# Optimization experiments

Hardware: AMD Instinct MI355X
Metric: run time of the kernel (lower is better)

## Reference

```python
import jax, jax.numpy as jnp
import numpy as np

T, N = 24, 2048
INPUT_DIM, HIDDEN, MEDIATE, SOCIAL, OUT_DIM = 2, 64, 128, 64, 2
N_SIZE = 2
CELL = 0.3
T_OBS, T_PRED = 9, 19
WIN = (N_SIZE + 1) ** 2  # (N_size+1)^2 = 9 window cells


def _social_pool(h, coords, mask):
    """Faithful social pooling for N_size=2, grid_cell_size=0.3.

    torch builds a dynamic grid, scatter-adds every agent's h into its cell,
    then gathers grid[int(x-R):int(x+R), int(y-R):int(y+R)] per agent.
    With R=0.3 and integer positions >= 4 (guaranteed by the margin), that
    slice is exactly the single cell (x-1, y-1), broadcast over the 3x3
    window. We compute it as a pairwise match without materializing a grid.
    Runs under torch.no_grad() -> stop_gradient.
    """
    margin = 2 * N_SIZE * CELL
    lt = jnp.stack([coords[:, 0].min(), coords[:, 1].min()]) - margin
    p = jnp.floor((coords - lt) / CELL).astype(jnp.int32)            # [N,2]
    p = p * mask.astype(jnp.int32)[:, None]                          # masked agents -> cell (0,0)
    q = p - 1                                                        # gathered cell per agent
    match = (p[None, :, 0] == q[:, None, 0]) & (p[None, :, 1] == q[:, None, 1])  # [i,j]
    cell_val = match.astype(h.dtype) @ h                             # [N,hidden] scatter-add + gather
    Hf = jnp.tile(cell_val, (1, WIN)) * mask[:, None]                # broadcast over 3x3 window, flat
    return jax.lax.stop_gradient(Hf)


def _forward(X, part_masks, all_h_t, all_c_t, Y, W_in, b_in, W_soc, b_soc,
             W_ih, W_hh, b_ih, b_hh, W_out, b_out, T_obs, T_pred):
    relu = jax.nn.relu  # dropout_prob = 0 -> Phi == ReLU

    def lstm(z, h, c):
        g = z @ W_ih.T + b_ih + h @ W_hh.T + b_hh
        i, f, gg, o = jnp.split(g, 4, axis=1)
        c = jax.nn.sigmoid(f) * c + jax.nn.sigmoid(i) * jnp.tanh(gg)
        h = jax.nn.sigmoid(o) * jnp.tanh(c)
        return h, c

    def cell_out(r, h, c, coords, m):
        Hf = _social_pool(h, coords, m)
        e = relu(Hf @ W_soc.T + b_soc)
        z = jnp.concatenate([r, e], axis=1)
        h, c = lstm(z, h, c)
        out = (h @ W_out.T + b_out) * m[:, None]
        return h, c, out

    def step_obs(carry, inp):
        h, c = carry
        x, m = inp
        r = relu(x @ W_in.T + b_in)
        h, c, out = cell_out(r, h, c, x, m)
        return (h, c), out

    (h, c), outs_obs = jax.lax.scan(
        step_obs, (all_h_t, all_c_t), (X[:T_obs + 1], part_masks[:T_obs + 1]))

    def step_pred(carry, inp):
        h, c, last_pt, prev_out = carry
        x, m = inp
        r = relu(last_pt @ W_in.T + b_in)
        h, c, out = cell_out(r, h, c, x, m)
        # torch: last_point = outputs[frame_idx - 1] AFTER the frame runs
        return (h, c, prev_out, out), out

    carry0 = (h, c, X[T_obs + 1], outs_obs[-1])
    _, outs_pred = jax.lax.scan(
        step_pred, carry0, (X[T_obs + 1:T_pred + 1], part_masks[T_obs + 1:T_pred + 1]))

    tail = jnp.zeros((X.shape[0] - T_pred - 1, X.shape[1], OUT_DIM), X.dtype)
    return jnp.concatenate([outs_obs, outs_pred, tail], axis=0)


def setup_inputs() -> dict:
    key = jax.random.key(0)
    ks = jax.random.split(key, 13)

    def lin(kw, kb, out_d, in_d):  # torch nn.Linear default init
        lim = 1.0 / float(np.sqrt(in_d))
        W = jax.random.uniform(kw, (out_d, in_d), minval=-lim, maxval=lim, dtype=jnp.float32)
        b = jax.random.uniform(kb, (out_d,), minval=-lim, maxval=lim, dtype=jnp.float32)
        return W, b

    W_in, b_in = lin(ks[0], ks[1], MEDIATE, INPUT_DIM)
    W_soc, b_soc = lin(ks[2], ks[3], SOCIAL, WIN * HIDDEN)
    W_ih, b_ih = lin(ks[4], ks[5], 4 * HIDDEN, MEDIATE + SOCIAL)
    W_hh, b_hh = lin(ks[6], ks[7], 4 * HIDDEN, HIDDEN)
    W_out, b_out = lin(ks[8], ks[9], OUT_DIM, HIDDEN)

    X = jax.random.normal(ks[10], (T, N, INPUT_DIM), dtype=jnp.float32) * 10.0  # meter-scale coords
    part_masks = (jax.random.uniform(ks[11], (T, N)) < 0.9).astype(jnp.float32)  # binary presence mask
    Y = jax.random.normal(ks[12], (T, N, INPUT_DIM), dtype=jnp.float32)  # unused by forward
    all_h_t = jnp.zeros((N, HIDDEN), jnp.float32)
    all_c_t = jnp.zeros((N, HIDDEN), jnp.float32)

    return {"X": X, "part_masks": part_masks, "all_h_t": all_h_t, "all_c_t": all_c_t,
            "Y": Y, "T_obs": T_OBS, "T_pred": T_PRED,
            "W_in": W_in, "b_in": b_in, "W_soc": W_soc, "b_soc": b_soc,
            "W_ih": W_ih, "W_hh": W_hh, "b_ih": b_ih, "b_hh": b_hh,
            "W_out": W_out, "b_out": b_out}


def reference(X, part_masks, all_h_t, all_c_t, Y, T_obs, T_pred,
              W_in, b_in, W_soc, b_soc, W_ih, W_hh, b_ih, b_hh, W_out, b_out):
    return _forward(X, part_masks, all_h_t, all_c_t, Y, W_in, b_in, W_soc, b_soc,
                    W_ih, W_hh, b_ih, b_hh, W_out, b_out, int(T_obs), int(T_pred))
```

## Files before the change

### kernel.cpp

```cpp
#include <hip/hip_runtime.h>
#include <math.h>


#define N_AG   2048
#define STEPS  20
#define CAP    12

typedef short short8 __attribute__((ext_vector_type(8)));
typedef float f32x4  __attribute__((ext_vector_type(4)));
union FU { uint4 q; short8 v; };

__device__ __forceinline__ unsigned short bf16rne(float x) {
    unsigned u = __float_as_uint(x);
    unsigned r = (u + 0x7fff + ((u >> 16) & 1)) >> 16;
    return (unsigned short)r;
}

__device__ __forceinline__ void pack8(const float* v, uint4& hq, uint4& lq) {
    unsigned uh[4], ul[4];
    #pragma unroll
    for (int w = 0; w < 4; w++) {
        float v0 = v[2 * w], v1 = v[2 * w + 1];
        unsigned short h0 = bf16rne(v0), h1 = bf16rne(v1);
        float f0 = __uint_as_float(((unsigned)h0) << 16);
        float f1 = __uint_as_float(((unsigned)h1) << 16);
        unsigned short l0 = bf16rne(v0 - f0), l1 = bf16rne(v1 - f1);
        uh[w] = (unsigned)h0 | ((unsigned)h1 << 16);
        ul[w] = (unsigned)l0 | ((unsigned)l1 << 16);
    }
    hq = make_uint4(uh[0], uh[1], uh[2], uh[3]);
    lq = make_uint4(ul[0], ul[1], ul[2], ul[3]);
}

__device__ __forceinline__ int khash(int k) {
    return (int)(((unsigned)k * 2654435761u) >> 21);
}

__device__ __forceinline__ float fsigm(float x) {
    return __builtin_amdgcn_rcpf(1.f + __expf(-x));
}
__device__ __forceinline__ float ftanh(float x) {
    float e = __expf(2.f * x);
    return 1.f - 2.f * __builtin_amdgcn_rcpf(e + 1.f);
}

__global__ __launch_bounds__(512) void k_pre(
    const float* __restrict__ X, const float* __restrict__ masks,
    const float* __restrict__ Wsoc,
    float* __restrict__ Wef, int* __restrict__ mcnt, int* __restrict__ midx,
    int* __restrict__ need, float* __restrict__ otail)
{
    const int bx = blockIdx.x, tid = threadIdx.x;

    if (bx >= 21) {
        otail[(bx - 21) * 512 + tid] = 0.f;
        return;
    }
    if (bx == 20) {
        for (int i = tid; i < 4096; i += 512) {
            int s = i >> 6, k = i & 63;
            float a = 0.f;
            #pragma unroll
            for (int w = 0; w < 9; w++) a += Wsoc[s * 576 + w * 64 + k];
            Wef[i] = a;
        }
        return;
    }

    __shared__ int kk[N_AG];
    __shared__ int head[N_AG];
    __shared__ int nxt[N_AG];
    __shared__ float red[512];
    const int t = bx;
    const float* Xt = X + t * N_AG * 2;

    float mnx = 1e30f, mny = 1e30f;
    for (int i = tid; i < N_AG; i += 512) {
        mnx = fminf(mnx, Xt[2 * i]);
        mny = fminf(mny, Xt[2 * i + 1]);
    }
    red[tid] = mnx; __syncthreads();
    for (int s = 256; s > 0; s >>= 1) { if (tid < s) red[tid] = fminf(red[tid], red[tid + s]); __syncthreads(); }
    float ltx = red[0]; __syncthreads();
    red[tid] = mny; __syncthreads();
    for (int s = 256; s > 0; s >>= 1) { if (tid < s) red[tid] = fminf(red[tid], red[tid + s]); __syncthreads(); }
    float lty = red[0]; __syncthreads();
    ltx -= 1.2f;
    lty -= 1.2f;

    for (int i = tid; i < N_AG; i += 512) {
        float m = masks[t * N_AG + i];
        int px = (int)floorf((Xt[2 * i]     - ltx) / 0.3f);
        int py = (int)floorf((Xt[2 * i + 1] - lty) / 0.3f);
        int im = (int)m;
        px *= im; py *= im;
        kk[i] = px * 65536 + py;
        head[i] = -1;
        if (t >= 1) need[(t - 1) * N_AG + i] = 0;
    }
    __syncthreads();
    for (int j = tid; j < N_AG; j += 512) {
        int kj = kk[j];
        if (kj != 0) nxt[j] = atomicExch(&head[khash(kj)], j);
    }
    __syncthreads();
    for (int i = tid; i < N_AG; i += 512) {
        int ki = kk[i];
        int cnt = 0;
        int base = (t * N_AG + i) * CAP;
        if (ki != 0) {
            int tkey = ki - 65537;
            int lst[CAP];
            for (int j = head[khash(tkey)]; j >= 0; j = nxt[j]) {
                if (kk[j] == tkey) { if (cnt < CAP) lst[cnt] = j; cnt++; }
            }
            if (cnt > CAP) cnt = CAP;
            for (int a = 1; a < cnt; a++) {
                int v = lst[a]; int b = a - 1;
                while (b >= 0 && lst[b] > v) { lst[b + 1] = lst[b]; b--; }
                lst[b + 1] = v;
            }
            for (int a = 0; a < cnt; a++) {
                midx[base + a] = lst[a];
                if (t >= 1) need[(t - 1) * N_AG + lst[a]] = 1;
            }
        }
        mcnt[t * N_AG + i] = cnt;
    }
}

struct KP {
    const float *X, *masks, *h_in, *c_in;
    const float *Win, *bin, *bsoc, *Wih, *Whh, *bih, *bhh, *Wout, *bout;
    const float *Wef;
    const int *mcnt, *midx, *need;
    float *out;
    unsigned long long *hist;
};

__global__ __launch_bounds__(512, 2) void k_persist(KP p)
{
    __shared__ __align__(16) uint4 zshq[544];
    __shared__ __align__(16) uint4 zslq[544];
    __shared__ float gbuf[16][258];
    __shared__ float cvs[16][64];
    __shared__ float hs[16][68];
    __shared__ float sWefP[64 * 65];
    __shared__ float2 sWinP[16 * 17];
    __shared__ float sBinP[16 * 9];
    __shared__ float sX[11][16][2];
    __shared__ float sMask[STEPS][16];
    __shared__ int   sCnt[STEPS][16];
    __shared__ int   sNeed[19][16];
    __shared__ int   sMidx[STEPS][16][CAP];
    __shared__ float sBsoc[64], sBc[256], sWout[128], sBout[2];
    __shared__ uint4 sE0h[8], sE0l[8];

    const int tid   = threadIdx.x;
    const int bx    = blockIdx.x;
    const int wbase = bx * 16;
    const int wv    = tid >> 6, lane = tid & 63;
    const int mA    = lane & 15, quad = lane >> 4;
    const int nt0   = 2 * wv;
    const int m0    = wv, m1 = wv + 8;

    if (tid < 256) sBc[tid] = p.bih[tid] + p.bhh[tid];
    if (tid < 128) {
        sWout[tid] = p.Wout[tid];
        int c = tid;
        sWinP[(c >> 3) * 17 + (c & 7)] = make_float2(p.Win[2 * c], p.Win[2 * c + 1]);
        sBinP[(c >> 3) * 9 + (c & 7)] = p.bin[c];
    }
    if (tid < 64) sBsoc[tid] = p.bsoc[tid];
    if (tid < 2)  sBout[tid] = p.bout[tid];
    if (tid < 8) {
        float v[8];
        #pragma unroll
        for (int j = 0; j < 8; j++) v[j] = fmaxf(p.bsoc[tid * 8 + j], 0.f);
        pack8(v, sE0h[tid], sE0l[tid]);
    }
    if (tid < 352) { int tt = tid / 32, r = tid % 32;
                     sX[tt][r >> 1][r & 1] = p.X[tt * (N_AG * 2) + (wbase + (r >> 1)) * 2 + (r & 1)]; }
    if (tid < 320) { int tt = tid / 16, m2 = tid % 16;
                     sMask[tt][m2] = p.masks[tt * N_AG + wbase + m2];
                     sCnt[tt][m2]  = p.mcnt[tt * N_AG + wbase + m2]; }
    if (tid < 304) { int s = tid / 16, m2 = tid % 16;
                     sNeed[s][m2] = p.need[s * N_AG + wbase + m2]; }
    for (int i = tid; i < 4096; i += 512) sWefP[(i >> 6) * 65 + (i & 63)] = p.Wef[i];
    for (int i = tid; i < STEPS * 16 * CAP; i += 512) {
        int tt = i / (16 * CAP), r = i % (16 * CAP), m2 = r / CAP, n = r % CAP;
        sMidx[tt][m2][n] = p.midx[(tt * N_AG + wbase + m2) * CAP + n];
    }

    float c0, c1;
    hs[m0][lane] = p.h_in[(wbase + m0) * 64 + lane];
    hs[m1][lane] = p.h_in[(wbase + m1) * 64 + lane];
    c0 = p.c_in[(wbase + m0) * 64 + lane];
    c1 = p.c_in[(wbase + m1) * 64 + lane];

    FU wh[2][8], wl[2][8];
    #pragma unroll
    for (int e = 0; e < 2; e++) {
        int g = (nt0 + e) * 16 + mA;
        #pragma unroll
        for (int kt = 0; kt < 8; kt++) {
            int k0 = kt * 32 + quad * 8;
            const float* src = (k0 < 192) ? (p.Wih + g * 192 + k0)
                                          : (p.Whh + g * 64 + (k0 - 192));
            float v[8];
            #pragma unroll
            for (int j = 0; j < 8; j++) v[j] = src[j];
            pack8(v, wh[e][kt].q, wl[e][kt].q);
        }
    }

    float oprev0x = 0.f, oprev0y = 0.f, oprev1x = 0.f, oprev1y = 0.f;

    __syncthreads();

    {
        if (lane < 32) {
            int a = lane & 1, s5r = lane >> 1;
            int m = a ? m1 : m0;
            float px = sX[0][m][0], py = sX[0][m][1];
            float v[8];
            #pragma unroll
            for (int j = 0; j < 8; j++) {
                float2 w2 = sWinP[s5r * 17 + j];
                v[j] = fmaxf(w2.x * px + w2.y * py + sBinP[s5r * 9 + j], 0.f);
            }
            pack8(v, zshq[s5r * 17 + m], zslq[s5r * 17 + m]);
        } else if (lane < 48) {
            int idx = lane - 32, a = idx & 1, s58 = idx >> 1;
            int m = a ? m1 : m0;
            float v[8];
            #pragma unroll
            for (int j = 0; j < 8; j++) v[j] = hs[m][s58 * 8 + j];
            pack8(v, zshq[(24 + s58) * 17 + m], zslq[(24 + s58) * 17 + m]);
        } else {
            int idx = lane - 48, a = idx & 1, s58 = idx >> 1;
            int m = a ? m1 : m0;
            if (sCnt[0][m] == 0) {
                zshq[(16 + s58) * 17 + m] = sE0h[s58];
                zslq[(16 + s58) * 17 + m] = sE0l[s58];
            }
        }
        #pragma unroll
        for (int a = 0; a < 2; a++) {
            int m = a ? m1 : m0;
            int cnt = sCnt[0][m];
            if (cnt > 0) {
                float cv = 0.f;
                for (int n = 0; n < cnt; n++)
                    cv += p.h_in[sMidx[0][m][n] * 64 + lane];
                cvs[m][lane] = cv;
                float acc = sBsoc[lane];
                const float* wp = &sWefP[lane * 65];
                #pragma unroll 8
                for (int k = 0; k < 64; k++) acc += cvs[m][k] * wp[k];
                acc = fmaxf(acc, 0.f);
                float v[8];
                #pragma unroll
                for (int jj = 0; jj < 8; jj++)
                    v[jj] = __shfl(acc, (lane & 7) * 8 + jj, 64);
                if (lane < 8)
                    pack8(v, zshq[(16 + lane) * 17 + m], zslq[(16 + lane) * 17 + m]);
            }
        }
    }
    __syncthreads();

    #pragma unroll 1
    for (int t = 0; t < STEPS; t++) {
        {
            f32x4 a0v = {0.f, 0.f, 0.f, 0.f};
            f32x4 a1v = {0.f, 0.f, 0.f, 0.f};
            #pragma unroll
            for (int kt = 0; kt < 8; kt++) {
                int fi = (kt * 4 + quad) * 17 + mA;
                FU az, bz;
                az.q = zshq[fi];
                bz.q = zslq[fi];
                a0v = __builtin_amdgcn_mfma_f32_16x16x32_bf16(az.v, wh[0][kt].v, a0v, 0, 0, 0);
                a1v = __builtin_amdgcn_mfma_f32_16x16x32_bf16(az.v, wh[1][kt].v, a1v, 0, 0, 0);
                a0v = __builtin_amdgcn_mfma_f32_16x16x32_bf16(bz.v, wh[0][kt].v, a0v, 0, 0, 0);
                a1v = __builtin_amdgcn_mfma_f32_16x16x32_bf16(bz.v, wh[1][kt].v, a1v, 0, 0, 0);
                a0v = __builtin_amdgcn_mfma_f32_16x16x32_bf16(az.v, wl[0][kt].v, a0v, 0, 0, 0);
                a1v = __builtin_amdgcn_mfma_f32_16x16x32_bf16(az.v, wl[1][kt].v, a1v, 0, 0, 0);
            }
            #pragma unroll
            for (int r = 0; r < 4; r++) {
                int row = quad * 4 + r;
                gbuf[row][nt0 * 16 + mA]       = a0v[r];
                gbuf[row][(nt0 + 1) * 16 + mA] = a1v[r];
            }
        }
        __syncthreads();

        {
            const int hid = lane;
            float hn0, hn1;
            {
                float gi = gbuf[m0][hid]       + sBc[hid];
                float gf = gbuf[m0][64 + hid]  + sBc[64 + hid];
                float gR = gbuf[m0][128 + hid] + sBc[128 + hid];
                float go = gbuf[m0][192 + hid] + sBc[192 + hid];
                float cn = fsigm(gf) * c0 + fsigm(gi) * ftanh(gR);
                hn0 = fsigm(go) * ftanh(cn);
                c0 = cn;
            }
            {
                float gi = gbuf[m1][hid]       + sBc[hid];
                float gf = gbuf[m1][64 + hid]  + sBc[64 + hid];
                float gR = gbuf[m1][128 + hid] + sBc[128 + hid];
                float go = gbuf[m1][192 + hid] + sBc[192 + hid];
                float cn = fsigm(gf) * c1 + fsigm(gi) * ftanh(gR);
                hn1 = fsigm(go) * ftanh(cn);
                c1 = cn;
            }
            if (t <= 18) {
                unsigned long long* hp = p.hist + (size_t)t * (N_AG * 64);
                unsigned long long tg = ((unsigned long long)(t + 1)) << 32;
                if (sNeed[t][m0])
                    __hip_atomic_store(&hp[(wbase + m0) * 64 + hid],
                                       tg | (unsigned long long)__float_as_uint(hn0),
                                       __ATOMIC_RELAXED, __HIP_MEMORY_SCOPE_AGENT);
                if (sNeed[t][m1])
                    __hip_atomic_store(&hp[(wbase + m1) * 64 + hid],
                                       tg | (unsigned long long)__float_as_uint(hn1),
                                       __ATOMIC_RELAXED, __HIP_MEMORY_SCOPE_AGENT);
            }
            hs[m0][hid] = hn0;
            hs[m1][hid] = hn1;

            float w0 = sWout[hid], w1 = sWout[64 + hid];
            float p00 = hn0 * w0, p01 = hn0 * w1;
            float p10 = hn1 * w0, p11 = hn1 * w1;
            #pragma unroll
            for (int off = 32; off >= 1; off >>= 1) {
                p00 += __shfl_xor(p00, off);
                p01 += __shfl_xor(p01, off);
                p10 += __shfl_xor(p10, off);
                p11 += __shfl_xor(p11, off);
            }
            float mk0 = sMask[t][m0], mk1 = sMask[t][m1];
            float o00 = (p00 + sBout[0]) * mk0, o01 = (p01 + sBout[1]) * mk0;
            float o10 = (p10 + sBout[0]) * mk1, o11 = (p11 + sBout[1]) * mk1;
            if (lane == 0)
                *(float2*)&p.out[(t * N_AG + wbase + m0) * 2] = make_float2(o00, o01);
            if (lane == 1)
                *(float2*)&p.out[(t * N_AG + wbase + m1) * 2] = make_float2(o10, o11);

            if (t < STEPS - 1) {
                const int tn = t + 1;
                if (lane < 32) {
                    int a = lane & 1, s5r = lane >> 1;
                    int m = a ? m1 : m0;
                    float px, py;
                    if (tn <= 10) { px = sX[tn][m][0]; py = sX[tn][m][1]; }
                    else          { px = a ? oprev1x : oprev0x;
                                    py = a ? oprev1y : oprev0y; }
                    float v[8];
                    #pragma unroll
                    for (int j = 0; j < 8; j++) {
                        float2 w2 = sWinP[s5r * 17 + j];
                        v[j] = fmaxf(w2.x * px + w2.y * py + sBinP[s5r * 9 + j], 0.f);
                    }
                    pack8(v, zshq[s5r * 17 + m], zslq[s5r * 17 + m]);
                } else if (lane < 48) {
                    int idx = lane - 32, a = idx & 1, s58 = idx >> 1;
                    int m = a ? m1 : m0;
                    float v[8];
                    #pragma unroll
                    for (int j = 0; j < 8; j++) v[j] = hs[m][s58 * 8 + j];
                    pack8(v, zshq[(24 + s58) * 17 + m], zslq[(24 + s58) * 17 + m]);
                } else {
                    int idx = lane - 48, a = idx & 1, s58 = idx >> 1;
                    int m = a ? m1 : m0;
                    if (sCnt[tn][m] == 0) {
                        zshq[(16 + s58) * 17 + m] = sE0h[s58];
                        zslq[(16 + s58) * 17 + m] = sE0l[s58];
                    }
                }
                #pragma unroll
                for (int a = 0; a < 2; a++) {
                    int m = a ? m1 : m0;
                    int cnt = sCnt[tn][m];
                    if (cnt > 0) {
                        const unsigned long long* hb =
                            p.hist + (size_t)t * (N_AG * 64);
                        const unsigned tagw = (unsigned)tn;
                        float cv = 0.f;
                        for (int n = 0; n < cnt; n++) {
                            int r = sMidx[tn][m][n];
                            unsigned long long wd;
                            do { wd = __hip_atomic_load(&hb[r * 64 + lane],
                                     __ATOMIC_RELAXED, __HIP_MEMORY_SCOPE_AGENT);
                            } while ((unsigned)(wd >> 32) != tagw);
                            cv += __uint_as_float((unsigned)wd);
                        }
                        cvs[m][lane] = cv;
                        float acc = sBsoc[lane];
                        const float* wp = &sWefP[lane * 65];
                        #pragma unroll 8
                        for (int k = 0; k < 64; k++) acc += cvs[m][k] * wp[k];
                        acc = fmaxf(acc, 0.f);
                        float v[8];
                        #pragma unroll
                        for (int jj = 0; jj < 8; jj++)
                            v[jj] = __shfl(acc, (lane & 7) * 8 + jj, 64);
                        if (lane < 8)
                            pack8(v, zshq[(16 + lane) * 17 + m],
                                     zslq[(16 + lane) * 17 + m]);
                    }
                }
            }
            oprev0x = o00; oprev0y = o01;
            oprev1x = o10; oprev1y = o11;
        }
        __syncthreads();
    }
}

extern "C" void kernel_launch(void* const* d_in, const int* in_sizes, int n_in,
                              void* d_out, int out_size, void* d_ws, size_t ws_size,
                              hipStream_t stream)
{
    KP kp;
    kp.X     = (const float*)d_in[0];
    kp.masks = (const float*)d_in[1];
    kp.h_in  = (const float*)d_in[2];
    kp.c_in  = (const float*)d_in[3];
    kp.Win   = (const float*)d_in[7];
    kp.bin   = (const float*)d_in[8];
    const float* Wsoc = (const float*)d_in[9];
    kp.bsoc  = (const float*)d_in[10];
    kp.Wih   = (const float*)d_in[11];
    kp.Whh   = (const float*)d_in[12];
    kp.bih   = (const float*)d_in[13];
    kp.bhh   = (const float*)d_in[14];
    kp.Wout  = (const float*)d_in[15];
    kp.bout  = (const float*)d_in[16];
    kp.out   = (float*)d_out;

    unsigned long long* hist = (unsigned long long*)d_ws;
    float* Wef = (float*)(hist + 19 * N_AG * 64);
    int*   need = (int*)(Wef + 4096);
    int*   mcnt = need + 19 * N_AG;
    int*   midx = mcnt + STEPS * N_AG;

    kp.hist = hist; kp.Wef = Wef; kp.need = need; kp.mcnt = mcnt; kp.midx = midx;

    k_pre<<<53, 512, 0, stream>>>(kp.X, kp.masks, Wsoc, Wef, mcnt, midx, need,
                                  kp.out + 20 * N_AG * 2);

    k_persist<<<128, 512, 0, stream>>>(kp);
}
```

Baseline: 195.6 us.

## Split LSTM gate GEMM so agents without neighbours finish before social gather

The per-step gate MFMA is split into a part that excludes the social-embedding K-tiles and a second part that adds them. Agents with no matched neighbours use a precomputed ReLU(b_soc)·W_ih term, so they finish their LSTM update and publish h early. The blocking neighbour gather then runs between the two halves instead of after output. Barriers become plain s_waitcnt lgkmcnt(0) plus s_barrier. The aim is to shorten the critical chain of cross-block spin-waits, at the cost of an extra barrier and gate buffer per step.

```diff
diff --git a/kernel.cpp b/kernel.cpp
--- a/kernel.cpp
+++ b/kernel.cpp
@@ -44,6 +44,10 @@
     return 1.f - 2.f * __builtin_amdgcn_rcpf(e + 1.f);
 }
 
+__device__ __forceinline__ void bar_lds() {
+    asm volatile("s_waitcnt lgkmcnt(0)\n\ts_barrier" ::: "memory");
+}
+
 __global__ __launch_bounds__(512) void k_pre(
     const float* __restrict__ X, const float* __restrict__ masks,
     const float* __restrict__ Wsoc,
@@ -142,7 +146,8 @@
 {
     __shared__ __align__(16) uint4 zshq[544];
     __shared__ __align__(16) uint4 zslq[544];
-    __shared__ float gbuf[16][258];
+    __shared__ float gbufA[16][258];
+    __shared__ float gbufB[16][258];
     __shared__ float cvs[16][64];
     __shared__ float hs[16][68];
     __shared__ float sWefP[64 * 65];
@@ -153,7 +158,7 @@
     __shared__ int   sCnt[STEPS][16];
     __shared__ int   sNeed[19][16];
     __shared__ int   sMidx[STEPS][16][CAP];
-    __shared__ float sBsoc[64], sBc[256], sWout[128], sBout[2];
+    __shared__ float sBsoc[64], sBc[256], sWout[128], sBout[2], sEW0[256];
     __shared__ uint4 sE0h[8], sE0l[8];
 
     const int tid   = threadIdx.x;
@@ -164,7 +169,13 @@
     const int nt0   = 2 * wv;
     const int m0    = wv, m1 = wv + 8;
 
-    if (tid < 256) sBc[tid] = p.bih[tid] + p.bhh[tid];
+    if (tid < 256) {
+        sBc[tid] = p.bih[tid] + p.bhh[tid];
+        float acc = 0.f;
+        const float* wp = p.Wih + tid * 192 + 128;
+        for (int k = 0; k < 64; k++) acc += fmaxf(p.bsoc[k], 0.f) * wp[k];
+        sEW0[tid] = acc;
+    }
     if (tid < 128) {
         sWout[tid] = p.Wout[tid];
         int c = tid;
@@ -245,87 +256,156 @@
                 zslq[(16 + s58) * 17 + m] = sE0l[s58];
             }
         }
-        #pragma unroll
-        for (int a = 0; a < 2; a++) {
-            int m = a ? m1 : m0;
-            int cnt = sCnt[0][m];
-            if (cnt > 0) {
-                float cv = 0.f;
-                for (int n = 0; n < cnt; n++)
-                    cv += p.h_in[sMidx[0][m][n] * 64 + lane];
-                cvs[m][lane] = cv;
-                float acc = sBsoc[lane];
-                const float* wp = &sWefP[lane * 65];
-                #pragma unroll 8
-                for (int k = 0; k < 64; k++) acc += cvs[m][k] * wp[k];
-                acc = fmaxf(acc, 0.f);
-                float v[8];
-                #pragma unroll
-                for (int jj = 0; jj < 8; jj++)
-                    v[jj] = __shfl(acc, (lane & 7) * 8 + jj, 64);
-                if (lane < 8)
-                    pack8(v, zshq[(16 + lane) * 17 + m], zslq[(16 + lane) * 17 + m]);
-            }
-        }
-    }
-    __syncthreads();
+    }
+    bar_lds();
 
     #pragma unroll 1
     for (int t = 0; t < STEPS; t++) {
-        {
-            f32x4 a0v = {0.f, 0.f, 0.f, 0.f};
-            f32x4 a1v = {0.f, 0.f, 0.f, 0.f};
-            #pragma unroll
-            for (int kt = 0; kt < 8; kt++) {
-                int fi = (kt * 4 + quad) * 17 + mA;
-                FU az, bz;
-                az.q = zshq[fi];
-                bz.q = zslq[fi];
-                a0v = __builtin_amdgcn_mfma_f32_16x16x32_bf16(az.v, wh[0][kt].v, a0v, 0, 0, 0);
-                a1v = __builtin_amdgcn_mfma_f32_16x16x32_bf16(az.v, wh[1][kt].v, a1v, 0, 0, 0);
-                a0v = __builtin_amdgcn_mfma_f32_16x16x32_bf16(bz.v, wh[0][kt].v, a0v, 0, 0, 0);
-                a1v = __builtin_amdgcn_mfma_f32_16x16x32_bf16(bz.v, wh[1][kt].v, a1v, 0, 0, 0);
-                a0v = __builtin_amdgcn_mfma_f32_16x16x32_bf16(az.v, wl[0][kt].v, a0v, 0, 0, 0);
-                a1v = __builtin_amdgcn_mfma_f32_16x16x32_bf16(az.v, wl[1][kt].v, a1v, 0, 0, 0);
-            }
-            #pragma unroll
-            for (int r = 0; r < 4; r++) {
-                int row = quad * 4 + r;
-                gbuf[row][nt0 * 16 + mA]       = a0v[r];
-                gbuf[row][(nt0 + 1) * 16 + mA] = a1v[r];
-            }
-        }
-        __syncthreads();
+        const bool mt0 = sCnt[t][m0] > 0;
+        const bool mt1 = sCnt[t][m1] > 0;
+        float hn0, hn1;
+
+        f32x4 a0v = {0.f, 0.f, 0.f, 0.f};
+        f32x4 a1v = {0.f, 0.f, 0.f, 0.f};
+        #pragma unroll
+        for (int u = 0; u < 6; u++) {
+            const int kt = (u < 4) ? u : u + 2;
+            int fi = (kt * 4 + quad) * 17 + mA;
+            FU az, bz;
+            az.q = zshq[fi];
+            bz.q = zslq[fi];
+            a0v = __builtin_amdgcn_mfma_f32_16x16x32_bf16(az.v, wh[0][kt].v, a0v, 0, 0, 0);
+            a1v = __builtin_amdgcn_mfma_f32_16x16x32_bf16(az.v, wh[1][kt].v, a1v, 0, 0, 0);
+            a0v = __builtin_amdgcn_mfma_f32_16x16x32_bf16(bz.v, wh[0][kt].v, a0v, 0, 0, 0);
+            a1v = __builtin_amdgcn_mfma_f32_16x16x32_bf16(bz.v, wh[1][kt].v, a1v, 0, 0, 0);
+            a0v = __builtin_amdgcn_mfma_f32_16x16x32_bf16(az.v, wl[0][kt].v, a0v, 0, 0, 0);
+            a1v = __builtin_amdgcn_mfma_f32_16x16x32_bf16(az.v, wl[1][kt].v, a1v, 0, 0, 0);
+        }
+        #pragma unroll
+        for (int r = 0; r < 4; r++) {
+            int row = quad * 4 + r;
+            gbufA[row][nt0 * 16 + mA]       = a0v[r];
+            gbufA[row][(nt0 + 1) * 16 + mA] = a1v[r];
+        }
+        bar_lds();
 
         {
             const int hid = lane;
-            float hn0, hn1;
-            {
-                float gi = gbuf[m0][hid]       + sBc[hid];
-                float gf = gbuf[m0][64 + hid]  + sBc[64 + hid];
-                float gR = gbuf[m0][128 + hid] + sBc[128 + hid];
-                float go = gbuf[m0][192 + hid] + sBc[192 + hid];
+            unsigned long long* hp = p.hist + (size_t)t * (N_AG * 64);
+            const unsigned long long tg = ((unsigned long long)(t + 1)) << 32;
+            if (!mt0) {
+                float gi = gbufA[m0][hid]       + sBc[hid]       + sEW0[hid];
+                float gf = gbufA[m0][64 + hid]  + sBc[64 + hid]  + sEW0[64 + hid];
+                float gR = gbufA[m0][128 + hid] + sBc[128 + hid] + sEW0[128 + hid];
+                float go = gbufA[m0][192 + hid] + sBc[192 + hid] + sEW0[192 + hid];
                 float cn = fsigm(gf) * c0 + fsigm(gi) * ftanh(gR);
                 hn0 = fsigm(go) * ftanh(cn);
                 c0 = cn;
-            }
-            {
-                float gi = gbuf[m1][hid]       + sBc[hid];
-                float gf = gbuf[m1][64 + hid]  + sBc[64 + hid];
-                float gR = gbuf[m1][128 + hid] + sBc[128 + hid];
-                float go = gbuf[m1][192 + hid] + sBc[192 + hid];
+                if (t <= 18 && sNeed[t][m0])
+                    __hip_atomic_store(&hp[(wbase + m0) * 64 + hid],
+                                       tg | (unsigned long long)__float_as_uint(hn0),
+                                       __ATOMIC_RELAXED, __HIP_MEMORY_SCOPE_AGENT);
+            }
+            if (!mt1) {
+                float gi = gbufA[m1][hid]       + sBc[hid]       + sEW0[hid];
+                float gf = gbufA[m1][64 + hid]  + sBc[64 + hid]  + sEW0[64 + hid];
+                float gR = gbufA[m1][128 + hid] + sBc[128 + hid] + sEW0[128 + hid];
+                float go = gbufA[m1][192 + hid] + sBc[192 + hid] + sEW0[192 + hid];
                 float cn = fsigm(gf) * c1 + fsigm(gi) * ftanh(gR);
                 hn1 = fsigm(go) * ftanh(cn);
                 c1 = cn;
-            }
-            if (t <= 18) {
-                unsigned long long* hp = p.hist + (size_t)t * (N_AG * 64);
-                unsigned long long tg = ((unsigned long long)(t + 1)) << 32;
-                if (sNeed[t][m0])
+                if (t <= 18 && sNeed[t][m1])
+                    __hip_atomic_store(&hp[(wbase + m1) * 64 + hid],
+                                       tg | (unsigned long long)__float_as_uint(hn1),
+                                       __ATOMIC_RELAXED, __HIP_MEMORY_SCOPE_AGENT);
+            }
+            #pragma unroll
+            for (int a = 0; a < 2; a++) {
+                int m = a ? m1 : m0;
+                int cnt = sCnt[t][m];
+                if (cnt > 0) {
+                    float cv = 0.f;
+                    if (t == 0) {
+                        for (int n = 0; n < cnt; n++)
+                            cv += p.h_in[sMidx[0][m][n] * 64 + lane];
+                    } else {
+                        const unsigned long long* hb =
+                            p.hist + (size_t)(t - 1) * (N_AG * 64);
+                        const unsigned tagw = (unsigned)t;
+                        for (int n = 0; n < cnt; n++) {
+                            int r = sMidx[t][m][n];
+                            unsigned long long wd;
+                            do { wd = __hip_atomic_load(&hb[r * 64 + lane],
+                                     __ATOMIC_RELAXED, __HIP_MEMORY_SCOPE_AGENT);
+                            } while ((unsigned)(wd >> 32) != tagw);
+                            cv += __uint_as_float((unsigned)wd);
+                        }
+                    }
+                    cvs[m][lane] = cv;
+                    float acc = sBsoc[lane];
+                    const float* wp = &sWefP[lane * 65];
+                    #pragma unroll 8
+                    for (int k = 0; k < 64; k++) acc += cvs[m][k] * wp[k];
+                    acc = fmaxf(acc, 0.f);
+                    float v[8];
+                    #pragma unroll
+                    for (int jj = 0; jj < 8; jj++)
+                        v[jj] = __shfl(acc, (lane & 7) * 8 + jj, 64);
+                    if (lane < 8)
+                        pack8(v, zshq[(16 + lane) * 17 + m],
+                                 zslq[(16 + lane) * 17 + m]);
+                }
+            }
+        }
+        bar_lds();
+
+        #pragma unroll
+        for (int kt = 4; kt <= 5; kt++) {
+            int fi = (kt * 4 + quad) * 17 + mA;
+            FU az, bz;
+            az.q = zshq[fi];
+            bz.q = zslq[fi];
+            a0v = __builtin_amdgcn_mfma_f32_16x16x32_bf16(az.v, wh[0][kt].v, a0v, 0, 0, 0);
+            a1v = __builtin_amdgcn_mfma_f32_16x16x32_bf16(az.v, wh[1][kt].v, a1v, 0, 0, 0);
+            a0v = __builtin_amdgcn_mfma_f32_16x16x32_bf16(bz.v, wh[0][kt].v, a0v, 0, 0, 0);
+            a1v = __builtin_amdgcn_mfma_f32_16x16x32_bf16(bz.v, wh[1][kt].v, a1v, 0, 0, 0);
+            a0v = __builtin_amdgcn_mfma_f32_16x16x32_bf16(az.v, wl[0][kt].v, a0v, 0, 0, 0);
+            a1v = __builtin_amdgcn_mfma_f32_16x16x32_bf16(az.v, wl[1][kt].v, a1v, 0, 0, 0);
+        }
+        #pragma unroll
+        for (int r = 0; r < 4; r++) {
+            int row = quad * 4 + r;
+            gbufB[row][nt0 * 16 + mA]       = a0v[r];
+            gbufB[row][(nt0 + 1) * 16 + mA] = a1v[r];
+        }
+        bar_lds();
+
+        {
+            const int hid = lane;
+            unsigned long long* hp = p.hist + (size_t)t * (N_AG * 64);
+            const unsigned long long tg = ((unsigned long long)(t + 1)) << 32;
+            if (mt0) {
+                float gi = gbufB[m0][hid]       + sBc[hid];
+                float gf = gbufB[m0][64 + hid]  + sBc[64 + hid];
+                float gR = gbufB[m0][128 + hid] + sBc[128 + hid];
+                float go = gbufB[m0][192 + hid] + sBc[192 + hid];
+                float cn = fsigm(gf) * c0 + fsigm(gi) * ftanh(gR);
+                hn0 = fsigm(go) * ftanh(cn);
+                c0 = cn;
+                if (t <= 18 && sNeed[t][m0])
                     __hip_atomic_store(&hp[(wbase + m0) * 64 + hid],
                                        tg | (unsigned long long)__float_as_uint(hn0),
                                        __ATOMIC_RELAXED, __HIP_MEMORY_SCOPE_AGENT);
-                if (sNeed[t][m1])
+            }
+            if (mt1) {
+                float gi = gbufB[m1][hid]       + sBc[hid];
+                float gf = gbufB[m1][64 + hid]  + sBc[64 + hid];
+                float gR = gbufB[m1][128 + hid] + sBc[128 + hid];
+                float go = gbufB[m1][192 + hid] + sBc[192 + hid];
+                float cn = fsigm(gf) * c1 + fsigm(gi) * ftanh(gR);
+                hn1 = fsigm(go) * ftanh(cn);
+                c1 = cn;
+                if (t <= 18 && sNeed[t][m1])
                     __hip_atomic_store(&hp[(wbase + m1) * 64 + hid],
                                        tg | (unsigned long long)__float_as_uint(hn1),
                                        __ATOMIC_RELAXED, __HIP_MEMORY_SCOPE_AGENT);
@@ -382,43 +462,11 @@
                         zslq[(16 + s58) * 17 + m] = sE0l[s58];
                     }
                 }
-                #pragma unroll
-                for (int a = 0; a < 2; a++) {
-                    int m = a ? m1 : m0;
-                    int cnt = sCnt[tn][m];
-                    if (cnt > 0) {
-                        const unsigned long long* hb =
-                            p.hist + (size_t)t * (N_AG * 64);
-                        const unsigned tagw = (unsigned)tn;
-                        float cv = 0.f;
-                        for (int n = 0; n < cnt; n++) {
-                            int r = sMidx[tn][m][n];
-                            unsigned long long wd;
-                            do { wd = __hip_atomic_load(&hb[r * 64 + lane],
-                                     __ATOMIC_RELAXED, __HIP_MEMORY_SCOPE_AGENT);
-                            } while ((unsigned)(wd >> 32) != tagw);
-                            cv += __uint_as_float((unsigned)wd);
-                        }
-                        cvs[m][lane] = cv;
-                        float acc = sBsoc[lane];
-                        const float* wp = &sWefP[lane * 65];
-                        #pragma unroll 8
-                        for (int k = 0; k < 64; k++) acc += cvs[m][k] * wp[k];
-                        acc = fmaxf(acc, 0.f);
-                        float v[8];
-                        #pragma unroll
-                        for (int jj = 0; jj < 8; jj++)
-                            v[jj] = __shfl(acc, (lane & 7) * 8 + jj, 64);
-                        if (lane < 8)
-                            pack8(v, zshq[(16 + lane) * 17 + m],
-                                     zslq[(16 + lane) * 17 + m]);
-                    }
-                }
             }
             oprev0x = o00; oprev0y = o01;
             oprev1x = o10; oprev1y = o11;
         }
-        __syncthreads();
+        bar_lds();
     }
 }
 
```

Result: slower. 204.4 us (+4.5%).
